# Kernel tuning notes

Measured on AMD Instinct MI355X. Metric: run time of the kernel, lower is better.

The kernel has to match this reference:

```python
import jax, jax.numpy as jnp
import numpy as np

B, S, R, H = 64, 2048, 1024, 512  # batch, att_size, rnn_size, att_hid_size


def setup_inputs() -> dict:
    key = jax.random.key(0)
    ks = jax.random.split(key, 8)
    h = jax.random.normal(ks[0], (B, R), dtype=jnp.float32)
    att_feats = jax.random.normal(ks[1], (B, S, R), dtype=jnp.float32)
    p_att_feats = jax.random.normal(ks[2], (B, S, H), dtype=jnp.float32)
    att_masks = jax.random.randint(ks[3], (B, S), 0, 2, dtype=jnp.int32)
    # h2att: Linear(rnn_size -> att_hid_size) with bias
    W_h2att = jax.random.normal(ks[4], (H, R), dtype=jnp.float32) / np.sqrt(R)
    b_h2att = jax.random.normal(ks[5], (H,), dtype=jnp.float32) * 0.01
    # alpha_net: Linear(att_hid_size -> 1) with bias
    w_alpha = jax.random.normal(ks[6], (H,), dtype=jnp.float32) / np.sqrt(H)
    b_alpha = jax.random.normal(ks[7], (), dtype=jnp.float32) * 0.01
    return {"h": h, "att_feats": att_feats, "p_att_feats": p_att_feats,
            "att_masks": att_masks, "W_h2att": W_h2att, "b_h2att": b_h2att,
            "w_alpha": w_alpha, "b_alpha": b_alpha}


def reference(h, att_feats, p_att_feats, att_masks, W_h2att, b_h2att, w_alpha, b_alpha):
    # att_h = h2att(h): [B, H]
    att_h = h @ W_h2att.T + b_h2att
    # dot = tanh(p_att_feats + att_h[:, None, :]): [B, S, H]  (ATT_ACT != 'RELU' -> Tanh; dropout disabled)
    dot = jnp.tanh(p_att_feats + att_h[:, None, :])
    # alpha_net to scalar per region: [B, S]
    scores = jnp.einsum('bsh,h->bs', dot, w_alpha) + b_alpha
    weight = jax.nn.softmax(scores, axis=1)
    # mask + renormalize
    m = att_masks.astype(weight.dtype)
    weight = weight * m
    weight = weight / jnp.sum(weight, axis=1, keepdims=True)
    # weighted sum of att_feats: [B, R]
    att_res = jnp.einsum('bs,bsr->br', weight, att_feats)
    return att_res
```

## Files before the change

### kernel.cpp

```cpp
#include <hip/hip_runtime.h>
#include <cstdint>
#include <cmath>

#define NB 64
#define NS 2048
#define NR 1024
#define NH 512
#define SC 32
#define SCHUNK (NS / SC)

__device__ __forceinline__ float waveReduceSum(float v) {
    #pragma unroll
    for (int off = 32; off > 0; off >>= 1) v += __shfl_down(v, off, 64);
    return v;
}

__device__ __forceinline__ float fast_tanh(float x) {
    float cx = fminf(fmaxf(x, -15.f), 15.f);
    float e = __expf(2.f * cx);
    return __fdividef(e - 1.f, e + 1.f);
}

__global__ __launch_bounds__(256) void k_atth(
    const float* __restrict__ h, const float* __restrict__ W,
    const float* __restrict__ bias, float* __restrict__ att_h,
    float* __restrict__ sums)
{
    const int o = blockIdx.x;
    if (o == 0 && threadIdx.x < NB) sums[threadIdx.x] = 0.f;
    __shared__ float wsh[NR];
    for (int i = threadIdx.x; i < NR; i += 256) wsh[i] = W[(size_t)o * NR + i];
    __syncthreads();
    const int wave = threadIdx.x >> 6, lane = threadIdx.x & 63;
    const float4* w4 = (const float4*)wsh;
    const float bo = bias[o];
    for (int b = wave; b < NB; b += 4) {
        const float4* h4 = (const float4*)(h + (size_t)b * NR);
        float acc = 0.f;
        #pragma unroll
        for (int i = 0; i < NR / 4 / 64; ++i) {
            float4 a = h4[lane + i * 64];
            float4 w = w4[lane + i * 64];
            acc += a.x * w.x + a.y * w.y + a.z * w.z + a.w * w.w;
        }
        acc = waveReduceSum(acc);
        if (lane == 0) att_h[b * NH + o] = acc + bo;
    }
}

__global__ __launch_bounds__(256) void k_scores(
    const float* __restrict__ p, const float* __restrict__ att_h,
    const float* __restrict__ w_alpha,
    const int* __restrict__ masks, float* __restrict__ weights,
    float* __restrict__ sums)
{
    const int b = blockIdx.x >> 7;
    const int s_base = (blockIdx.x & 127) << 4;
    const int wave = threadIdx.x >> 6, lane = threadIdx.x & 63;
    __shared__ float ah[NH], wa[NH];
    __shared__ int cidx[16];
    __shared__ int nnz_s;
    __shared__ float blksum;
    if (threadIdx.x == 0) blksum = 0.f;
    for (int i = threadIdx.x; i < NH; i += 256) {
        ah[i] = att_h[b * NH + i];
        wa[i] = w_alpha[i];
    }
    if (threadIdx.x < 64) {
        bool on = false;
        if (threadIdx.x < 16) on = (masks[b * NS + s_base + threadIdx.x] != 0);
        unsigned long long m = __ballot(on);
        if (threadIdx.x < 16) {
            if (on) {
                int my = (int)__popcll(m & ((1ull << threadIdx.x) - 1ull));
                cidx[my] = threadIdx.x;
            } else {
                weights[b * NS + s_base + threadIdx.x] = 0.f;
            }
        }
        if (threadIdx.x == 0) nnz_s = (int)__popcll(m);
    }
    __syncthreads();
    const int nnz = nnz_s;
    const float4* ah4 = (const float4*)ah;
    const float4* wa4 = (const float4*)wa;
    float esum = 0.f;
    for (int i = wave; i < nnz; i += 4) {
        const int s = s_base + cidx[i];
        const int sidx = b * NS + s;
        const float4* p4 = (const float4*)(p + (size_t)sidx * NH);
        float4 x0 = p4[lane];
        float4 x1 = p4[lane + 64];
        float4 a0 = ah4[lane],      a1 = ah4[lane + 64];
        float4 w0 = wa4[lane],      w1 = wa4[lane + 64];
        float acc = 0.f;
        acc += fast_tanh(x0.x + a0.x) * w0.x;
        acc += fast_tanh(x0.y + a0.y) * w0.y;
        acc += fast_tanh(x0.z + a0.z) * w0.z;
        acc += fast_tanh(x0.w + a0.w) * w0.w;
        acc += fast_tanh(x1.x + a1.x) * w1.x;
        acc += fast_tanh(x1.y + a1.y) * w1.y;
        acc += fast_tanh(x1.z + a1.z) * w1.z;
        acc += fast_tanh(x1.w + a1.w) * w1.w;
        acc = waveReduceSum(acc);
        if (lane == 0) {
            float e = __expf(fminf(acc, 60.f));
            weights[sidx] = e;
            esum += e;
        }
    }
    if (lane == 0 && esum != 0.f) atomicAdd(&blksum, esum);
    __syncthreads();
    if (threadIdx.x == 0 && blksum != 0.f) atomicAdd(&sums[b], blksum);
}

__global__ __launch_bounds__(256) void k_wsum(
    const float* __restrict__ feats, const float* __restrict__ weights,
    const float* __restrict__ sums, float* __restrict__ out)
{
    const int b  = blockIdx.x >> 5;
    const int sc = blockIdx.x & 31;
    const int s0 = sc * SCHUNK;
    __shared__ float cw[SCHUNK];
    __shared__ int   cidx[SCHUNK];
    __shared__ int   nnz_s;
    if (threadIdx.x < 64) {
        float w = weights[b * NS + s0 + threadIdx.x];
        unsigned long long m = __ballot(w != 0.f);
        if (w != 0.f) {
            int my = (int)__popcll(m & ((1ull << threadIdx.x) - 1ull));
            cw[my] = w; cidx[my] = threadIdx.x;
        }
        if (threadIdx.x == 0) nnz_s = (int)__popcll(m);
    }
    __syncthreads();
    const int nnz = nnz_s;
    const float invT = 1.0f / sums[b];
    const float4* f4 = (const float4*)(feats + ((size_t)b * NS + s0) * NR);
    float4 acc = make_float4(0.f, 0.f, 0.f, 0.f);
    int i = 0;
    for (; i + 4 <= nnz; i += 4) {
        const float w0 = cw[i], w1 = cw[i + 1], w2 = cw[i + 2], w3 = cw[i + 3];
        const float4 v0 = f4[(size_t)cidx[i    ] * 256 + threadIdx.x];
        const float4 v1 = f4[(size_t)cidx[i + 1] * 256 + threadIdx.x];
        const float4 v2 = f4[(size_t)cidx[i + 2] * 256 + threadIdx.x];
        const float4 v3 = f4[(size_t)cidx[i + 3] * 256 + threadIdx.x];
        acc.x += w0 * v0.x + w1 * v1.x + w2 * v2.x + w3 * v3.x;
        acc.y += w0 * v0.y + w1 * v1.y + w2 * v2.y + w3 * v3.y;
        acc.z += w0 * v0.z + w1 * v1.z + w2 * v2.z + w3 * v3.z;
        acc.w += w0 * v0.w + w1 * v1.w + w2 * v2.w + w3 * v3.w;
    }
    for (; i < nnz; ++i) {
        const float w = cw[i];
        const float4 v = f4[(size_t)cidx[i] * 256 + threadIdx.x];
        acc.x += w * v.x; acc.y += w * v.y; acc.z += w * v.z; acc.w += w * v.w;
    }
    float* o = out + b * NR + threadIdx.x * 4;
    atomicAdd(o + 0, acc.x * invT);
    atomicAdd(o + 1, acc.y * invT);
    atomicAdd(o + 2, acc.z * invT);
    atomicAdd(o + 3, acc.w * invT);
}

extern "C" void kernel_launch(void* const* d_in, const int* in_sizes, int n_in,
                              void* d_out, int out_size, void* d_ws, size_t ws_size,
                              hipStream_t stream) {
    const float* h        = (const float*)d_in[0];
    const float* feats    = (const float*)d_in[1];
    const float* p        = (const float*)d_in[2];
    const int*   masks    = (const int*)d_in[3];
    const float* W        = (const float*)d_in[4];
    const float* bh       = (const float*)d_in[5];
    const float* w_alpha  = (const float*)d_in[6];
    float* out = (float*)d_out;

    float* ws      = (float*)d_ws;
    float* att_h   = ws;
    float* weights = att_h + NB * NH;
    float* sums    = weights + NB * NS;

    hipMemsetAsync(d_out, 0, (size_t)out_size * sizeof(float), stream);

    k_atth<<<NH, 256, 0, stream>>>(h, W, bh, att_h, sums);
    k_scores<<<NB * (NS / 16), 256, 0, stream>>>(p, att_h, w_alpha, masks, weights, sums);
    k_wsum<<<NB * SC, 256, 0, stream>>>(feats, weights, sums, out);
}
```

Measured before the change: 813.4 us.

## Fuse score and weighted-sum kernels, replace atomics with partial-sum reduction

Merges the score computation and the weighted feature sum into one kernel per (batch, 64-position chunk). Exponentiated scores stay in shared memory instead of going through a global weights buffer. Each block writes its partial result and its partial exp-sum to a workspace, and a small reduction kernel normalises and writes the output. This removes the output memset, the global atomics and one launch. In exchange, the 2048 fused blocks are now larger and more serialized, and an extra partial buffer is written and read back.

```diff
diff --git a/kernel.cpp b/kernel.cpp
--- a/kernel.cpp
+++ b/kernel.cpp
@@ -23,11 +23,9 @@
 
 __global__ __launch_bounds__(256) void k_atth(
     const float* __restrict__ h, const float* __restrict__ W,
-    const float* __restrict__ bias, float* __restrict__ att_h,
-    float* __restrict__ sums)
+    const float* __restrict__ bias, float* __restrict__ att_h)
 {
     const int o = blockIdx.x;
-    if (o == 0 && threadIdx.x < NB) sums[threadIdx.x] = 0.f;
     __shared__ float wsh[NR];
     for (int i = threadIdx.x; i < NR; i += 256) wsh[i] = W[(size_t)o * NR + i];
     __syncthreads();
@@ -48,35 +46,30 @@
     }
 }
 
-__global__ __launch_bounds__(256) void k_scores(
+__global__ __launch_bounds__(256) void k_fused(
     const float* __restrict__ p, const float* __restrict__ att_h,
-    const float* __restrict__ w_alpha,
-    const int* __restrict__ masks, float* __restrict__ weights,
-    float* __restrict__ sums)
+    const float* __restrict__ w_alpha, const int* __restrict__ masks,
+    const float* __restrict__ feats, float* __restrict__ partial,
+    float* __restrict__ esums)
 {
-    const int b = blockIdx.x >> 7;
-    const int s_base = (blockIdx.x & 127) << 4;
+    const int b  = blockIdx.x >> 5;
+    const int sc = blockIdx.x & 31;
+    const int s0 = sc * SCHUNK;
     const int wave = threadIdx.x >> 6, lane = threadIdx.x & 63;
     __shared__ float ah[NH], wa[NH];
-    __shared__ int cidx[16];
-    __shared__ int nnz_s;
-    __shared__ float blksum;
-    if (threadIdx.x == 0) blksum = 0.f;
+    __shared__ float cw[SCHUNK];
+    __shared__ int   cidx[SCHUNK];
+    __shared__ int   nnz_s;
     for (int i = threadIdx.x; i < NH; i += 256) {
         ah[i] = att_h[b * NH + i];
         wa[i] = w_alpha[i];
     }
     if (threadIdx.x < 64) {
-        bool on = false;
-        if (threadIdx.x < 16) on = (masks[b * NS + s_base + threadIdx.x] != 0);
+        bool on = (masks[b * NS + s0 + threadIdx.x] != 0);
         unsigned long long m = __ballot(on);
-        if (threadIdx.x < 16) {
-            if (on) {
-                int my = (int)__popcll(m & ((1ull << threadIdx.x) - 1ull));
-                cidx[my] = threadIdx.x;
-            } else {
-                weights[b * NS + s_base + threadIdx.x] = 0.f;
-            }
+        if (on) {
+            int my = (int)__popcll(m & ((1ull << threadIdx.x) - 1ull));
+            cidx[my] = threadIdx.x;
         }
         if (threadIdx.x == 0) nnz_s = (int)__popcll(m);
     }
@@ -84,11 +77,10 @@
     const int nnz = nnz_s;
     const float4* ah4 = (const float4*)ah;
     const float4* wa4 = (const float4*)wa;
-    float esum = 0.f;
+
     for (int i = wave; i < nnz; i += 4) {
-        const int s = s_base + cidx[i];
-        const int sidx = b * NS + s;
-        const float4* p4 = (const float4*)(p + (size_t)sidx * NH);
+        const int s = s0 + cidx[i];
+        const float4* p4 = (const float4*)(p + ((size_t)b * NS + s) * NH);
         float4 x0 = p4[lane];
         float4 x1 = p4[lane + 64];
         float4 a0 = ah4[lane],      a1 = ah4[lane + 64];
@@ -103,39 +95,16 @@
         acc += fast_tanh(x1.z + a1.z) * w1.z;
         acc += fast_tanh(x1.w + a1.w) * w1.w;
         acc = waveReduceSum(acc);
-        if (lane == 0) {
-            float e = __expf(fminf(acc, 60.f));
-            weights[sidx] = e;
-            esum += e;
-        }
-    }
-    if (lane == 0 && esum != 0.f) atomicAdd(&blksum, esum);
-    __syncthreads();
-    if (threadIdx.x == 0 && blksum != 0.f) atomicAdd(&sums[b], blksum);
-}
-
-__global__ __launch_bounds__(256) void k_wsum(
-    const float* __restrict__ feats, const float* __restrict__ weights,
-    const float* __restrict__ sums, float* __restrict__ out)
-{
-    const int b  = blockIdx.x >> 5;
-    const int sc = blockIdx.x & 31;
-    const int s0 = sc * SCHUNK;
-    __shared__ float cw[SCHUNK];
-    __shared__ int   cidx[SCHUNK];
-    __shared__ int   nnz_s;
-    if (threadIdx.x < 64) {
-        float w = weights[b * NS + s0 + threadIdx.x];
-        unsigned long long m = __ballot(w != 0.f);
-        if (w != 0.f) {
-            int my = (int)__popcll(m & ((1ull << threadIdx.x) - 1ull));
-            cw[my] = w; cidx[my] = threadIdx.x;
-        }
-        if (threadIdx.x == 0) nnz_s = (int)__popcll(m);
+        if (lane == 0) cw[i] = __expf(fminf(acc, 60.f));
     }
     __syncthreads();
-    const int nnz = nnz_s;
-    const float invT = 1.0f / sums[b];
+
+    if (threadIdx.x < 64) {
+        float e = (threadIdx.x < nnz) ? cw[threadIdx.x] : 0.f;
+        e = waveReduceSum(e);
+        if (threadIdx.x == 0) esums[b * SC + sc] = e;
+    }
+
     const float4* f4 = (const float4*)(feats + ((size_t)b * NS + s0) * NR);
     float4 acc = make_float4(0.f, 0.f, 0.f, 0.f);
     int i = 0;
@@ -155,11 +124,32 @@
         const float4 v = f4[(size_t)cidx[i] * 256 + threadIdx.x];
         acc.x += w * v.x; acc.y += w * v.y; acc.z += w * v.z; acc.w += w * v.w;
     }
-    float* o = out + b * NR + threadIdx.x * 4;
-    atomicAdd(o + 0, acc.x * invT);
-    atomicAdd(o + 1, acc.y * invT);
-    atomicAdd(o + 2, acc.z * invT);
-    atomicAdd(o + 3, acc.w * invT);
+    float4* o = (float4*)(partial + (size_t)(b * SC + sc) * NR);
+    o[threadIdx.x] = acc;
+}
+
+__global__ __launch_bounds__(64) void k_reduce(
+    const float* __restrict__ partial, const float* __restrict__ esums,
+    float* __restrict__ out)
+{
+    const int b    = blockIdx.x >> 2;
+    const int q    = blockIdx.x & 3;
+    const int lane = threadIdx.x;
+    float e = (lane < SC) ? esums[b * SC + lane] : 0.f;
+    float T = waveReduceSum(e);
+    T = __shfl(T, 0, 64);
+    const float invT = 1.0f / T;
+    const int r4 = q * 64 + lane;
+    const float4* p4 = (const float4*)(partial + (size_t)b * SC * NR);
+    float4 acc = make_float4(0.f, 0.f, 0.f, 0.f);
+    #pragma unroll 8
+    for (int c = 0; c < SC; ++c) {
+        float4 v = p4[(size_t)c * 256 + r4];
+        acc.x += v.x; acc.y += v.y; acc.z += v.z; acc.w += v.w;
+    }
+    float4 r;
+    r.x = acc.x * invT; r.y = acc.y * invT; r.z = acc.z * invT; r.w = acc.w * invT;
+    ((float4*)(out + (size_t)b * NR))[r4] = r;
 }
 
 extern "C" void kernel_launch(void* const* d_in, const int* in_sizes, int n_in,
@@ -176,12 +166,10 @@
 
     float* ws      = (float*)d_ws;
     float* att_h   = ws;
-    float* weights = att_h + NB * NH;
-    float* sums    = weights + NB * NS;
+    float* partial = att_h + NB * NH;
+    float* esums   = partial + (size_t)NB * SC * NR;
 
-    hipMemsetAsync(d_out, 0, (size_t)out_size * sizeof(float), stream);
-
-    k_atth<<<NH, 256, 0, stream>>>(h, W, bh, att_h, sums);
-    k_scores<<<NB * (NS / 16), 256, 0, stream>>>(p, att_h, w_alpha, masks, weights, sums);
-    k_wsum<<<NB * SC, 256, 0, stream>>>(feats, weights, sums, out);
+    k_atth  <<<NH,      256, 0, stream>>>(h, W, bh, att_h);
+    k_fused <<<NB * SC, 256, 0, stream>>>(p, att_h, w_alpha, masks, feats, partial, esums);
+    k_reduce<<<NB * 4,  64,  0, stream>>>(partial, esums, out);
 }
```

Result: faster. 786.9 us (-3.3%).
